# Kernel tuning notes

Hardware: AMD Instinct MI355X
Metric: run time of the kernel (lower is better)

Reference implementation:

```python
import jax, jax.numpy as jnp
import numpy as np
from jax import lax

D_MODEL = 1024
D_STATE = 128
D_CONV = 4
EXPAND = 2
HEADDIM = 64
D_INNER = EXPAND * D_MODEL          # 2048
NHEADS = D_INNER // HEADDIM         # 32
D_IN_PROJ = 2 * D_INNER + 2 * D_STATE + NHEADS  # 4384 (z, xBC, dt)
CONV_CH = D_INNER + 2 * D_STATE     # 2304
CHUNK = 128
EPS = 1e-5
BATCH, SEQ = 2, 2048


def silu(x):
    return x * jax.nn.sigmoid(x)


def rmsnorm(x, w):
    return x * lax.rsqrt(jnp.mean(x * x, axis=-1, keepdims=True) + EPS) * w


def segsum(a):
    # a: (b,h,c,q) -> (b,h,c,q,q); [i,j] = sum_{j<k<=i} a_k, -inf above diag
    q = a.shape[-1]
    cs = jnp.cumsum(a, axis=-1)
    seg = cs[..., :, None] - cs[..., None, :]
    mask = jnp.tril(jnp.ones((q, q), dtype=bool))
    return jnp.where(mask, seg, -jnp.inf)


def ssd(xh, dt, A, B, C):
    # xh: (b,l,h,p), dt: (b,l,h), A: (h,), B,C: (b,l,n). Chunked SSD scan.
    b, l, h, p = xh.shape
    n = B.shape[-1]
    c = l // CHUNK
    X = (xh * dt[..., None]).reshape(b, c, CHUNK, h, p)
    Adt = (A * dt).reshape(b, c, CHUNK, h).transpose(0, 3, 1, 2)  # (b,h,c,q)
    Bc = B.reshape(b, c, CHUNK, n)
    Cc = C.reshape(b, c, CHUNK, n)
    Acs = jnp.cumsum(Adt, axis=-1)
    L = jnp.exp(segsum(Adt))  # (b,h,c,q,q) causal decay within chunk
    Y_diag = jnp.einsum('bcln,bcsn,bhcls,bcshp->bclhp', Cc, Bc, L, X)
    decay_states = jnp.exp(Acs[..., -1:] - Acs)
    states = jnp.einsum('bcln,bhcl,bclhp->bchpn', Bc, decay_states, X)
    chunk_decay = jnp.exp(Acs[..., -1])  # (b,h,c)

    def step(s, inp):
        st, cd = inp
        return s * cd[:, :, None, None] + st, s

    init = jnp.zeros((b, h, p, n), dtype=xh.dtype)
    _, prev = lax.scan(step, init,
                       (states.transpose(1, 0, 2, 3, 4), chunk_decay.transpose(2, 0, 1)))
    # prev: (c,b,h,p,n) = state at start of each chunk
    Y_off = jnp.einsum('bcln,cbhpn,bhcl->bclhp', Cc, prev, jnp.exp(Acs))
    return (Y_diag + Y_off).reshape(b, l, h, p)


def mamba2(x, in_w, conv_w, conv_b, dt_bias, A_log, D, gnorm_w, out_w):
    b, l, _ = x.shape
    zxbcdt = x @ in_w.T  # (b,l,D_IN_PROJ)
    z = zxbcdt[..., :D_INNER]
    xBC = zxbcdt[..., D_INNER:D_INNER + CONV_CH]
    dt = jax.nn.softplus(zxbcdt[..., D_INNER + CONV_CH:] + dt_bias)  # (b,l,h)
    # causal depthwise conv1d
    xp = jnp.pad(xBC, ((0, 0), (D_CONV - 1, 0), (0, 0)))
    conv = sum(xp[:, k:k + l, :] * conv_w[:, k] for k in range(D_CONV)) + conv_b
    xBC = silu(conv)
    xs = xBC[..., :D_INNER]
    B = xBC[..., D_INNER:D_INNER + D_STATE]
    C = xBC[..., D_INNER + D_STATE:]
    A = -jnp.exp(A_log)
    xh = xs.reshape(b, l, NHEADS, HEADDIM)
    y = ssd(xh, dt, A, B, C) + xh * D[None, None, :, None]
    y = y.reshape(b, l, D_INNER)
    y = rmsnorm(y * silu(z), gnorm_w)  # RMSNormGated
    return y @ out_w.T


def setup_inputs() -> dict:
    key = jax.random.key(0)
    ks = jax.random.split(key, 24)
    d = {}
    d['x'] = jax.random.normal(ks[0], (BATCH, SEQ, D_MODEL), dtype=jnp.float32)
    d['norm_w'] = jnp.ones((D_MODEL,), jnp.float32)
    d['out_w_blk'] = jax.random.normal(ks[1], (D_MODEL, 2 * D_MODEL), jnp.float32) * 0.02
    d['out_b_blk'] = jnp.zeros((D_MODEL,), jnp.float32)
    for i, pfx in enumerate(['f_', 'b_']):
        o = 2 + i * 10
        d[pfx + 'in_w'] = jax.random.normal(ks[o], (D_IN_PROJ, D_MODEL), jnp.float32) * 0.02
        d[pfx + 'conv_w'] = jax.random.normal(ks[o + 1], (CONV_CH, D_CONV), jnp.float32) * 0.2
        d[pfx + 'conv_b'] = jnp.zeros((CONV_CH,), jnp.float32)
        d[pfx + 'dt_bias'] = jax.random.normal(ks[o + 2], (NHEADS,), jnp.float32) * 0.1
        d[pfx + 'A_log'] = jnp.log(jax.random.uniform(ks[o + 3], (NHEADS,), jnp.float32, 1.0, 16.0))
        d[pfx + 'D'] = jnp.ones((NHEADS,), jnp.float32)
        d[pfx + 'gnorm_w'] = jnp.ones((D_INNER,), jnp.float32)
        d[pfx + 'out_w'] = jax.random.normal(ks[o + 4], (D_MODEL, D_INNER), jnp.float32) * 0.02
    return d


def reference(x, norm_w, out_w_blk, out_b_blk,
              f_in_w, f_conv_w, f_conv_b, f_dt_bias, f_A_log, f_D, f_gnorm_w, f_out_w,
              b_in_w, b_conv_w, b_conv_b, b_dt_bias, b_A_log, b_D, b_gnorm_w, b_out_w):
    xn = rmsnorm(x, norm_w)
    y_fwd = mamba2(xn, f_in_w, f_conv_w, f_conv_b, f_dt_bias, f_A_log, f_D, f_gnorm_w, f_out_w)
    y_bwd = jnp.flip(
        mamba2(jnp.flip(xn, axis=1), b_in_w, b_conv_w, b_conv_b, b_dt_bias, b_A_log, b_D, b_gnorm_w, b_out_w),
        axis=1)
    out = jnp.concatenate([y_fwd, y_bwd], axis=-1) @ out_w_blk.T + out_b_blk
    return x + out
```

## Files before the change

kernel.cpp:

```cpp
#include <hip/hip_runtime.h>
#include <hip/hip_bf16.h>
#include <math.h>

#define BATCH 2
#define SEQL 2048
#define T 4096
#define DMODEL 1024
#define DINNER 2048
#define DSTATE 128
#define NH 32
#define HD 64
#define DPROJ2 4352
#define CONVCH 2304
#define NCH 16
#define CHUNK 128
#define EPS 1e-5f

#define N_INW ((size_t)DPROJ2 * DMODEL)
#define N_OUTW ((size_t)DMODEL * DINNER)
#define N_ST ((size_t)BATCH * NCH * NH * HD * DSTATE)
#define F2B_BLOCKS 10752
#define TW_BLOCKS 1024

typedef unsigned short u16;
typedef __bf16 bf16x8 __attribute__((ext_vector_type(8)));
typedef float f32x4 __attribute__((ext_vector_type(4)));

__device__ __forceinline__ u16 f2b(float f) {
    union { float f; unsigned u; } v; v.f = f;
    unsigned r = v.u + 0x7fffu + ((v.u >> 16) & 1u);
    return (u16)(r >> 16);
}
__device__ __forceinline__ float b2f(u16 b) {
    union { unsigned u; float f; } v; v.u = ((unsigned)b) << 16;
    return v.f;
}
__device__ __forceinline__ int flipseq(int r) {
    return (r & ~(SEQL - 1)) | ((SEQL - 1) - (r & (SEQL - 1)));
}
__device__ __forceinline__ void gload16(const u16* g, u16* l) {
    __builtin_amdgcn_global_load_lds(
        (const __attribute__((address_space(1))) void*)g,
        (__attribute__((address_space(3))) void*)l, 16, 0, 0);
}

__device__ __forceinline__ float blockReduceSum(float v) {
    __shared__ float red_[4];
    for (int off = 32; off > 0; off >>= 1) v += __shfl_down(v, off);
    int lane = threadIdx.x & 63, wid = threadIdx.x >> 6;
    if (lane == 0) red_[wid] = v;
    __syncthreads();
    if (threadIdx.x == 0) {
        float s = 0.f;
        int nw = blockDim.x >> 6;
        for (int i = 0; i < nw; ++i) s += red_[i];
        red_[0] = s;
    }
    __syncthreads();
    return red_[0];
}

__global__ __launch_bounds__(256) void k_rmsnorm(
    const float* __restrict__ x, const float* __restrict__ w,
    u16* __restrict__ outb)
{
    int row = blockIdx.x;
    const float* xr = x + (size_t)row * DMODEL;
    float ss = 0.f;
    for (int i = threadIdx.x; i < DMODEL; i += 256) { float v = xr[i]; ss += v * v; }
    float tot = blockReduceSum(ss);
    float sc = rsqrtf(tot / DMODEL + EPS);
    for (int i = threadIdx.x; i < DMODEL; i += 256)
        outb[(size_t)row * DMODEL + i] = f2b(xr[i] * sc * w[i]);
}

__global__ __launch_bounds__(256) void k_wprep(
    const float* __restrict__ f_in_w, const float* __restrict__ b_in_w,
    const float* __restrict__ out_w_blk,
    const float* __restrict__ f_out_w, const float* __restrict__ b_out_w,
    u16* __restrict__ d_inwb, u16* __restrict__ d_owbb, u16* __restrict__ d_fowT)
{
    __shared__ u16 t[64][65];
    int bid = blockIdx.x;
    if (bid < F2B_BLOCKS) {
        size_t i = ((size_t)bid * 256 + threadIdx.x) * 4;
        const float* s; u16* d; size_t off;
        if (i < 2 * N_INW) {
            int dir = i >= N_INW;
            off = i - (size_t)dir * N_INW;
            s = dir ? b_in_w : f_in_w; d = d_inwb + (size_t)dir * N_INW;
        } else {
            off = i - 2 * N_INW;
            if (off >= N_OUTW) return;
            s = out_w_blk; d = d_owbb;
        }
        float4 v = *(const float4*)(s + off);
        ushort4 o;
        o.x = f2b(v.x); o.y = f2b(v.y); o.z = f2b(v.z); o.w = f2b(v.w);
        *(ushort4*)(d + off) = o;
        return;
    }
    int b2 = bid - F2B_BLOCKS;
    int dir = b2 >> 9;
    int rem = b2 & 511;
    int c0 = (rem & 31) * 64, e0 = (rem >> 5) * 64;
    const float* src = dir ? b_out_w : f_out_w;
    u16* d = d_fowT + (size_t)dir * N_OUTW;
    for (int i = threadIdx.x; i < 64 * 16; i += 256) {
        int el = i >> 4, c4 = (i & 15) * 4;
        float4 v = *(const float4*)(src + (size_t)(e0 + el) * DINNER + c0 + c4);
        t[c4 + 0][el] = f2b(v.x); t[c4 + 1][el] = f2b(v.y);
        t[c4 + 2][el] = f2b(v.z); t[c4 + 3][el] = f2b(v.w);
    }
    __syncthreads();
    for (int i = threadIdx.x; i < 64 * 16; i += 256) {
        int cl = i >> 4, e4 = (i & 15) * 4;
        ushort4 o;
        o.x = t[cl][e4]; o.y = t[cl][e4 + 1]; o.z = t[cl][e4 + 2]; o.w = t[cl][e4 + 3];
        *(ushort4*)(d + (size_t)(c0 + cl) * DMODEL + e0 + e4) = o;
    }
}

__global__ __launch_bounds__(256, 4) void k_mm_in(
    const u16* __restrict__ A, const u16* __restrict__ W0,
    u16* __restrict__ zb0, u16* __restrict__ xbcraw0)
{
    const int K = DMODEL;
    int dir = blockIdx.z;
    const u16* W = W0 + (size_t)dir * N_INW;
    int m0 = blockIdx.x * 128, n0 = blockIdx.y * 128;

    u16* Cout;
    int ldcc, nbase;
    if (n0 < DINNER) {
        Cout = zb0 + (size_t)dir * T * DINNER;
        ldcc = DINNER;
        nbase = n0;
    } else {
        Cout = xbcraw0 + (size_t)dir * T * CONVCH;
        ldcc = CONVCH;
        nbase = n0 - DINNER;
    }

    __shared__ u16 As[2 * 128 * 32];
    __shared__ u16 Bs[2 * 128 * 32];
    int tid = threadIdx.x;
    int lane = tid & 63;
    int wrow = ((tid >> 6) & 1) * 64, wcol = (tid >> 7) * 64;

    int srow = tid >> 2, skof = (tid & 3) * 8;
    int ar1 = m0 + srow, ar2 = ar1 + 64;
    if (dir) { ar1 = flipseq(ar1); ar2 = flipseq(ar2); }
    const u16* ga1 = A + (size_t)ar1 * K + skof;
    const u16* ga2 = A + (size_t)ar2 * K + skof;
    const u16* gb1 = W + (size_t)(n0 + srow) * K + skof;
    const u16* gb2 = gb1 + (size_t)64 * K;
    u16* la1 = As + tid * 8;
    u16* la2 = As + 2048 + tid * 8;
    u16* lb1 = Bs + tid * 8;
    u16* lb2 = Bs + 2048 + tid * 8;

    int aoff[4], boff[4];
    #pragma unroll
    for (int i = 0; i < 4; ++i) {
        aoff[i] = (wrow + i * 16 + (lane & 15)) * 32 + ((lane >> 4) * 8);
        boff[i] = (wcol + i * 16 + (lane & 15)) * 32 + ((lane >> 4) * 8);
    }

    f32x4 acc[4][4] = {};
    for (int kt = 0; kt < K; kt += 64) {
        gload16(ga1, la1);        gload16(ga2, la2);
        gload16(ga1 + 32, la1 + 4096); gload16(ga2 + 32, la2 + 4096);
        gload16(gb1, lb1);        gload16(gb2, lb2);
        gload16(gb1 + 32, lb1 + 4096); gload16(gb2 + 32, lb2 + 4096);
        ga1 += 64; ga2 += 64; gb1 += 64; gb2 += 64;
        __syncthreads();
        #pragma unroll
        for (int ks = 0; ks < 2; ++ks) {
            bf16x8 af[4], bfv[4];
            #pragma unroll
            for (int i = 0; i < 4; ++i) af[i] = *(const bf16x8*)(As + ks * 4096 + aoff[i]);
            #pragma unroll
            for (int j = 0; j < 4; ++j) bfv[j] = *(const bf16x8*)(Bs + ks * 4096 + boff[j]);
            #pragma unroll
            for (int i = 0; i < 4; ++i)
                #pragma unroll
                for (int j = 0; j < 4; ++j)
                    acc[i][j] = __builtin_amdgcn_mfma_f32_16x16x32_bf16(af[i], bfv[j], acc[i][j], 0, 0, 0);
        }
        __syncthreads();
    }

    int rbase = m0 + wrow + ((lane >> 4) << 2);
    int cbase = nbase + wcol + (lane & 15);
    #pragma unroll
    for (int i = 0; i < 4; ++i)
        #pragma unroll
        for (int j = 0; j < 4; ++j)
            #pragma unroll
            for (int r = 0; r < 4; ++r)
                Cout[(size_t)(rbase + i * 16 + r) * ldcc + cbase + j * 16] = f2b(acc[i][j][r]);
}

__global__ __launch_bounds__(256) void k_mm64(
    const u16* __restrict__ A0, const u16* __restrict__ W0,
    u16* __restrict__ Cb)
{
    int dir = blockIdx.z;
    const u16* A = A0 + dir * DMODEL;
    const u16* W = W0 + (size_t)dir * N_OUTW;

    __shared__ u16 As[2 * 128 * 32];
    __shared__ u16 Bs[2 * 64 * 32];
    int tid = threadIdx.x;
    int lane = tid & 63;
    int w = tid >> 6;
    int m0 = blockIdx.y * 128, n0 = blockIdx.x * 64;
    int wrow = (w & 1) * 64, wcol = (w >> 1) * 32;

    int srow = tid >> 2, skof = (tid & 3) * 8;
    const u16* ga1 = A + (size_t)(m0 + srow) * 2048 + skof;
    const u16* ga2 = A + (size_t)(m0 + 64 + srow) * 2048 + skof;
    const u16* gb  = W + (size_t)(n0 + srow) * DMODEL + skof;
    u16* la1 = As + tid * 8;
    u16* la2 = As + 2048 + tid * 8;
    u16* lb  = Bs + tid * 8;

    int aoff[4], boff[2];
    #pragma unroll
    for (int i = 0; i < 4; ++i)
        aoff[i] = (wrow + i * 16 + (lane & 15)) * 32 + ((lane >> 4) * 8);
    #pragma unroll
    for (int j = 0; j < 2; ++j)
        boff[j] = (wcol + j * 16 + (lane & 15)) * 32 + ((lane >> 4) * 8);

    f32x4 acc[4][2] = {};
    for (int kt = 0; kt < DMODEL; kt += 64) {
        gload16(ga1, la1); gload16(ga1 + 32, la1 + 4096);
        gload16(ga2, la2); gload16(ga2 + 32, la2 + 4096);
        gload16(gb, lb);   gload16(gb + 32, lb + 2048);
        ga1 += 64; ga2 += 64; gb += 64;
        __syncthreads();
        #pragma unroll
        for (int ks = 0; ks < 2; ++ks) {
            bf16x8 af[4], bfv[2];
            #pragma unroll
            for (int i = 0; i < 4; ++i) af[i] = *(const bf16x8*)(As + ks * 4096 + aoff[i]);
            #pragma unroll
            for (int j = 0; j < 2; ++j) bfv[j] = *(const bf16x8*)(Bs + ks * 2048 + boff[j]);
            #pragma unroll
            for (int i = 0; i < 4; ++i)
                #pragma unroll
                for (int j = 0; j < 2; ++j)
                    acc[i][j] = __builtin_amdgcn_mfma_f32_16x16x32_bf16(af[i], bfv[j], acc[i][j], 0, 0, 0);
        }
        __syncthreads();
    }

    int rbase = m0 + wrow + ((lane >> 4) << 2);
    int cbase = n0 + wcol + (lane & 15);
    #pragma unroll
    for (int i = 0; i < 4; ++i)
        #pragma unroll
        for (int j = 0; j < 2; ++j)
            #pragma unroll
            for (int r = 0; r < 4; ++r)
                Cb[(size_t)(rbase + i * 16 + r) * 4096 + dir * 2048 + cbase + j * 16] = f2b(acc[i][j][r]);
}

__global__ __launch_bounds__(256) void k_mm_fin(
    const u16* __restrict__ A1, const u16* __restrict__ A2,
    const u16* __restrict__ W,
    float* __restrict__ out, const float* __restrict__ bias,
    const float* __restrict__ resid)
{
    __shared__ u16 As[4 * 128 * 32];
    __shared__ u16 Bs[2 * 2 * 64 * 32];
    int tid = threadIdx.x;
    int lane = tid & 63;
    int w = tid >> 6;
    int m0 = blockIdx.y * 128, n0 = blockIdx.x * 64;
    int wrow = (w & 1) * 64, wcol = (w >> 1) * 32;

    int srow = tid >> 2, skof = (tid & 3) * 8;
    const u16* ga1  = A1 + (size_t)(m0 + srow) * DINNER + skof;
    const u16* ga1b = A1 + (size_t)(m0 + 64 + srow) * DINNER + skof;
    const u16* ga2  = A2 + (size_t)flipseq(m0 + srow) * DINNER + skof;
    const u16* ga2b = A2 + (size_t)flipseq(m0 + 64 + srow) * DINNER + skof;
    const u16* gb1 = W + (size_t)(n0 + srow) * 4096 + skof;
    const u16* gb2 = gb1 + 2048;
    u16* la1  = As + tid * 8;
    u16* la1b = As + 2048 + tid * 8;
    u16* la2  = As + 8192 + tid * 8;
    u16* la2b = As + 8192 + 2048 + tid * 8;
    u16* lb1 = Bs + tid * 8;
    u16* lb2 = Bs + 4096 + tid * 8;

    int aoff[4], boff[2];
    #pragma unroll
    for (int i = 0; i < 4; ++i)
        aoff[i] = (wrow + i * 16 + (lane & 15)) * 32 + ((lane >> 4) * 8);
    #pragma unroll
    for (int j = 0; j < 2; ++j)
        boff[j] = (wcol + j * 16 + (lane & 15)) * 32 + ((lane >> 4) * 8);

    f32x4 acc[4][2] = {};
    for (int kt = 0; kt < DINNER; kt += 64) {
        gload16(ga1, la1);    gload16(ga1 + 32, la1 + 4096);
        gload16(ga1b, la1b);  gload16(ga1b + 32, la1b + 4096);
        gload16(ga2, la2);    gload16(ga2 + 32, la2 + 4096);
        gload16(ga2b, la2b);  gload16(ga2b + 32, la2b + 4096);
        gload16(gb1, lb1);    gload16(gb1 + 32, lb1 + 2048);
        gload16(gb2, lb2);    gload16(gb2 + 32, lb2 + 2048);
        ga1 += 64; ga1b += 64; ga2 += 64; ga2b += 64; gb1 += 64; gb2 += 64;
        __syncthreads();
        #pragma unroll
        for (int h = 0; h < 2; ++h) {
            #pragma unroll
            for (int ks = 0; ks < 2; ++ks) {
                bf16x8 af[4], bfv[2];
                #pragma unroll
                for (int i = 0; i < 4; ++i)
                    af[i] = *(const bf16x8*)(As + h * 8192 + ks * 4096 + aoff[i]);
                #pragma unroll
                for (int j = 0; j < 2; ++j)
                    bfv[j] = *(const bf16x8*)(Bs + h * 4096 + ks * 2048 + boff[j]);
                #pragma unroll
                for (int i = 0; i < 4; ++i)
                    #pragma unroll
                    for (int j = 0; j < 2; ++j)
                        acc[i][j] = __builtin_amdgcn_mfma_f32_16x16x32_bf16(af[i], bfv[j], acc[i][j], 0, 0, 0);
            }
        }
        __syncthreads();
    }

    int rbase = m0 + wrow + ((lane >> 4) << 2);
    int cbase = n0 + wcol + (lane & 15);
    #pragma unroll
    for (int i = 0; i < 4; ++i)
        #pragma unroll
        for (int j = 0; j < 2; ++j)
            #pragma unroll
            for (int r = 0; r < 4; ++r) {
                int row = rbase + i * 16 + r, col = cbase + j * 16;
                out[(size_t)row * DMODEL + col] =
                    acc[i][j][r] + bias[col] + resid[(size_t)row * DMODEL + col];
            }
}

__global__ __launch_bounds__(256) void k_dt2(
    const u16* __restrict__ xnb,
    const float* __restrict__ inw_f, const float* __restrict__ inw_b,
    const float* __restrict__ dtb_f, const float* __restrict__ dtb_b,
    float* __restrict__ dt)
{
    int dir = blockIdx.z;
    const float* wbase = dir ? inw_b : inw_f;
    const float* dtbia = dir ? dtb_b : dtb_f;
    float* dtp = dt + (size_t)dir * T * NH;

    int r0 = blockIdx.x * 4;
    __shared__ float xs[4][1024];
    int tid = threadIdx.x;
    #pragma unroll
    for (int rr = 0; rr < 4; ++rr) {
        int src = dir ? flipseq(r0 + rr) : (r0 + rr);
        ushort4 v = *(const ushort4*)(xnb + (size_t)src * DMODEL + tid * 4);
        xs[rr][tid * 4 + 0] = b2f(v.x); xs[rr][tid * 4 + 1] = b2f(v.y);
        xs[rr][tid * 4 + 2] = b2f(v.z); xs[rr][tid * 4 + 3] = b2f(v.w);
    }
    __syncthreads();
    int h = tid >> 3, part = tid & 7;
    const float* w = wbase + (size_t)(DPROJ2 + h) * DMODEL;
    float a0 = 0.f, a1 = 0.f, a2 = 0.f, a3 = 0.f;
    for (int kk = 0; kk < 128; ++kk) {
        int k = part + (kk << 3);
        float wv = w[k];
        a0 += xs[0][k] * wv; a1 += xs[1][k] * wv;
        a2 += xs[2][k] * wv; a3 += xs[3][k] * wv;
    }
    #pragma unroll
    for (int off = 4; off > 0; off >>= 1) {
        a0 += __shfl_down(a0, off, 8); a1 += __shfl_down(a1, off, 8);
        a2 += __shfl_down(a2, off, 8); a3 += __shfl_down(a3, off, 8);
    }
    if (part == 0) {
        float bsh = dtbia[h];
        float vv[4] = {a0, a1, a2, a3};
        #pragma unroll
        for (int rr = 0; rr < 4; ++rr) {
            float v = vv[rr] + bsh;
            dtp[(size_t)(r0 + rr) * NH + h] = (v > 20.f) ? v : log1pf(expf(v));
        }
    }
}

__global__ void k_conv(const u16* __restrict__ xraw0,
                       const float* __restrict__ cw_f, const float* __restrict__ cw_b,
                       const float* __restrict__ cb_f, const float* __restrict__ cb_b,
                       const float* __restrict__ dt0,
                       u16* __restrict__ xbcb0, u16* __restrict__ xdtb0)
{
    int dir = blockIdx.z;
    const u16* xraw = xraw0 + (size_t)dir * T * CONVCH;
    const float* cw = dir ? cw_b : cw_f;
    const float* cb = dir ? cb_b : cb_f;
    const float* dt = dt0 + (size_t)dir * T * NH;
    u16* xbcb = xbcb0 + (size_t)dir * T * CONVCH;
    u16* xdtb = xdtb0 + (size_t)dir * T * DINNER;

    int idx = blockIdx.x * blockDim.x + threadIdx.x;
    if (idx >= (T / 4) * (CONVCH / 8)) return;
    int r4 = idx / (CONVCH / 8);
    int c8 = (idx - r4 * (CONVCH / 8)) * 8;
    int r0 = r4 * 4;
    int t0 = r0 & (SEQL - 1);

    float4 cwv[8];
    #pragma unroll
    for (int j = 0; j < 8; ++j) cwv[j] = *(const float4*)(cw + (size_t)(c8 + j) * 4);
    float acc[4][8];
    {
        float4 c0 = *(const float4*)(cb + c8);
        float4 c1 = *(const float4*)(cb + c8 + 4);
        #pragma unroll
        for (int i = 0; i < 4; ++i) {
            acc[i][0] = c0.x; acc[i][1] = c0.y; acc[i][2] = c0.z; acc[i][3] = c0.w;
            acc[i][4] = c1.x; acc[i][5] = c1.y; acc[i][6] = c1.z; acc[i][7] = c1.w;
        }
    }
    #pragma unroll
    for (int s = 0; s < 7; ++s) {
        int tt = t0 - 3 + s;
        if (tt < 0) continue;
        const u16* src = xraw + (size_t)(r0 - 3 + s) * CONVCH + c8;
        ushort4 v0 = *(const ushort4*)src;
        ushort4 v1 = *(const ushort4*)(src + 4);
        float xv[8] = {b2f(v0.x), b2f(v0.y), b2f(v0.z), b2f(v0.w),
                       b2f(v1.x), b2f(v1.y), b2f(v1.z), b2f(v1.w)};
        #pragma unroll
        for (int i = 0; i < 4; ++i) {
            if (i <= s && i >= s - 3) {
                const int j = s - i;
                #pragma unroll
                for (int ch = 0; ch < 8; ++ch) {
                    float wv = (j == 0) ? cwv[ch].x : (j == 1) ? cwv[ch].y
                             : (j == 2) ? cwv[ch].z : cwv[ch].w;
                    acc[i][ch] += xv[ch] * wv;
                }
            }
        }
    }
    #pragma unroll
    for (int i = 0; i < 4; ++i) {
        int r = r0 + i;
        float sgl[8];
        #pragma unroll
        for (int ch = 0; ch < 8; ++ch) sgl[ch] = acc[i][ch] / (1.f + __expf(-acc[i][ch]));
        ushort4 o0, o1;
        o0.x = f2b(sgl[0]); o0.y = f2b(sgl[1]); o0.z = f2b(sgl[2]); o0.w = f2b(sgl[3]);
        o1.x = f2b(sgl[4]); o1.y = f2b(sgl[5]); o1.z = f2b(sgl[6]); o1.w = f2b(sgl[7]);
        *(ushort4*)(xbcb + (size_t)r * CONVCH + c8) = o0;
        *(ushort4*)(xbcb + (size_t)r * CONVCH + c8 + 4) = o1;
        if (c8 < DINNER) {
            float dv = dt[(size_t)r * NH + (c8 >> 6)];
            ushort4 d0, d1;
            d0.x = f2b(sgl[0] * dv); d0.y = f2b(sgl[1] * dv);
            d0.z = f2b(sgl[2] * dv); d0.w = f2b(sgl[3] * dv);
            d1.x = f2b(sgl[4] * dv); d1.y = f2b(sgl[5] * dv);
            d1.z = f2b(sgl[6] * dv); d1.w = f2b(sgl[7] * dv);
            *(ushort4*)(xdtb + (size_t)r * DINNER + c8) = d0;
            *(ushort4*)(xdtb + (size_t)r * DINNER + c8 + 4) = d1;
        }
    }
}

#define LDW 136
__global__ __launch_bounds__(256) void k_states(
    const u16* __restrict__ xbcb0, const u16* __restrict__ xdtb0,
    const float* __restrict__ dt0,
    const float* __restrict__ Alog_f, const float* __restrict__ Alog_b,
    float* __restrict__ acs0, float* __restrict__ cd0, u16* __restrict__ st0)
{
    int dir = blockIdx.z;
    const u16* xbcb = xbcb0 + (size_t)dir * T * CONVCH;
    const u16* xdtb = xdtb0 + (size_t)dir * T * DINNER;
    const float* dt = dt0 + (size_t)dir * T * NH;
    const float* A_log = dir ? Alog_b : Alog_f;
    float* acs = acs0 + (size_t)dir * BATCH * NH * NCH * CHUNK;
    float* cd = cd0 + (size_t)dir * BATCH * NH * NCH;
    u16* st = st0 + (size_t)dir * N_ST;

    __shared__ u16 Bt[128 * LDW];
    __shared__ u16 Xt[64 * LDW];
    __shared__ float cs[128];
    __shared__ float dec_s[128];
    int tid = threadIdx.x;
    int lane = tid & 63;
    int w = tid >> 6;
    int h = blockIdx.x & 31;
    int bc = blockIdx.x >> 5;
    int c = bc & 15, b = bc >> 4;
    int row0 = b * SEQL + c * CHUNK;

    if (tid < 128) {
        float Ah = -expf(A_log[h]);
        cs[tid] = Ah * dt[(size_t)(row0 + tid) * NH + h];
    }
    for (int i = tid; i < 128 * 16; i += 256) {
        int l = i >> 4, pg = (i & 15) * 4;
        ushort4 v = *(const ushort4*)(xdtb + (size_t)(row0 + l) * DINNER + h * HD + pg);
        Xt[(pg + 0) * LDW + l] = v.x; Xt[(pg + 1) * LDW + l] = v.y;
        Xt[(pg + 2) * LDW + l] = v.z; Xt[(pg + 3) * LDW + l] = v.w;
    }
    __syncthreads();
    for (int off = 1; off < 128; off <<= 1) {
        float tval = 0.f;
        if (tid < 128 && tid >= off) tval = cs[tid - off];
        __syncthreads();
        if (tid < 128) cs[tid] += tval;
        __syncthreads();
    }
    size_t abase = ((size_t)(b * NH + h) * NCH + c) << 7;
    if (tid < 128) acs[abase + tid] = cs[tid];
    float a_last = cs[127];
    if (tid == 127) cd[(b * NH + h) * NCH + c] = expf(a_last);
    if (tid < 128) dec_s[tid] = __expf(a_last - cs[tid]);
    __syncthreads();
    for (int i = tid; i < 128 * 32; i += 256) {
        int l = i >> 5, ng = (i & 31) * 4;
        ushort4 v = *(const ushort4*)(xbcb + (size_t)(row0 + l) * CONVCH + DINNER + ng);
        float d = dec_s[l];
        Bt[(ng + 0) * LDW + l] = f2b(b2f(v.x) * d);
        Bt[(ng + 1) * LDW + l] = f2b(b2f(v.y) * d);
        Bt[(ng + 2) * LDW + l] = f2b(b2f(v.z) * d);
        Bt[(ng + 3) * LDW + l] = f2b(b2f(v.w) * d);
    }
    __syncthreads();
    f32x4 tacc[8] = {};
    for (int kk = 0; kk < 4; ++kk) {
        bf16x8 afs = *(const bf16x8*)(Xt + (w * 16 + (lane & 15)) * LDW
                                      + kk * 32 + (lane >> 4) * 8);
        #pragma unroll
        for (int j = 0; j < 8; ++j) {
            bf16x8 bfs = *(const bf16x8*)(Bt + (j * 16 + (lane & 15)) * LDW
                                          + kk * 32 + (lane >> 4) * 8);
            tacc[j] = __builtin_amdgcn_mfma_f32_16x16x32_bf16(afs, bfs, tacc[j], 0, 0, 0);
        }
    }
    size_t sb = (size_t)blockIdx.x * (HD * DSTATE);
    #pragma unroll
    for (int j = 0; j < 8; ++j)
        #pragma unroll
        for (int r = 0; r < 4; ++r) {
            int p = w * 16 + (lane >> 4) * 4 + r;
            int n = j * 16 + (lane & 15);
            st[sb + (size_t)p * DSTATE + n] = f2b(tacc[j][r]);
        }
}

__global__ void k_scan(u16* __restrict__ st0, const float* __restrict__ cd0)
{
    int i = blockIdx.x * blockDim.x + threadIdx.x;
    if (i >= 2 * BATCH * NH * HD * DSTATE) return;
    int dir = i >> 19;
    int j = i & ((1 << 19) - 1);
    u16* st = st0 + (size_t)dir * N_ST;
    const float* cd = cd0 + (size_t)dir * BATCH * NH * NCH;
    int n = j & 127;
    int rest = j >> 7;
    int p = rest & 63; rest >>= 6;
    int h = rest & 31;
    int b = rest >> 5;
    float s = 0.f;
    for (int c = 0; c < NCH; ++c) {
        size_t idx = ((size_t)((b * NCH + c) * NH + h) * HD + p) * DSTATE + n;
        float v = b2f(st[idx]);
        st[idx] = f2b(s);
        s = s * cd[(b * NH + h) * NCH + c] + v;
    }
}

__global__ __launch_bounds__(256) void k_chunk(
    const u16* __restrict__ xbcb0, const u16* __restrict__ xdtb0,
    const float* __restrict__ acs0, const u16* __restrict__ prev0,
    const float* __restrict__ D_f, const float* __restrict__ D_b,
    u16* __restrict__ y0)
{
    int dir = blockIdx.z;
    const u16* xbcb = xbcb0 + (size_t)dir * T * CONVCH;
    const u16* xdtb = xdtb0 + (size_t)dir * T * DINNER;
    const float* acs = acs0 + (size_t)dir * BATCH * NH * NCH * CHUNK;
    const u16* prev = prev0 + (size_t)dir * N_ST;
    const float* Dp = dir ? D_b : D_f;
    u16* y = y0 + (size_t)dir * T * DINNER;

    __shared__ u16 S0[128 * LDW];
    __shared__ u16 Xt[64 * LDW];
    __shared__ float acs_s[128];
    int tid = threadIdx.x;
    int lane = tid & 63;
    int w = tid >> 6;
    int h = blockIdx.x & 31;
    int bc = blockIdx.x >> 5;
    int c = bc & 15, b = bc >> 4;
    int row0 = b * SEQL + c * CHUNK;

    if (tid < 128)
        acs_s[tid] = acs[(((size_t)(b * NH + h) * NCH + c) << 7) + tid];
    for (int i = tid; i < 128 * 16; i += 256) {
        int s = i >> 4, m8 = (i & 15) * 8;
        *(uint4*)(S0 + s * LDW + m8) =
            *(const uint4*)(xbcb + (size_t)(row0 + s) * CONVCH + DINNER + m8);
    }
    for (int i = tid; i < 128 * 16; i += 256) {
        int l = i >> 4, pg = (i & 15) * 4;
        ushort4 v = *(const ushort4*)(xdtb + (size_t)(row0 + l) * DINNER + h * HD + pg);
        Xt[(pg + 0) * LDW + l] = v.x; Xt[(pg + 1) * LDW + l] = v.y;
        Xt[(pg + 2) * LDW + l] = v.z; Xt[(pg + 3) * LDW + l] = v.w;
    }
    __syncthreads();

    int wrow = (w & 1) * 64, wcol = (w >> 1) * 64;
    const u16* cbase = xbcb + (size_t)row0 * CONVCH + DINNER + DSTATE;
    f32x4 sacc[4][4] = {};
    for (int kk = 0; kk < 4; ++kk) {
        bf16x8 af[4], bfr[4];
        #pragma unroll
        for (int i = 0; i < 4; ++i)
            af[i] = *(const bf16x8*)(cbase + (size_t)(wrow + i * 16 + (lane & 15)) * CONVCH
                                     + kk * 32 + (lane >> 4) * 8);
        #pragma unroll
        for (int j = 0; j < 4; ++j)
            bfr[j] = *(const bf16x8*)(S0 + (wcol + j * 16 + (lane & 15)) * LDW
                                      + kk * 32 + (lane >> 4) * 8);
        #pragma unroll
        for (int i = 0; i < 4; ++i)
            #pragma unroll
            for (int j = 0; j < 4; ++j)
                if (wcol + j * 16 <= wrow + i * 16 + 15)
                    sacc[i][j] = __builtin_amdgcn_mfma_f32_16x16x32_bf16(af[i], bfr[j], sacc[i][j], 0, 0, 0);
    }
    __syncthreads();
    #pragma unroll
    for (int i = 0; i < 4; ++i)
        #pragma unroll
        for (int j = 0; j < 4; ++j) {
            int s = wcol + j * 16 + (lane & 15);
            #pragma unroll
            for (int r = 0; r < 4; ++r) {
                int l = wrow + i * 16 + (lane >> 4) * 4 + r;
                float v = (s <= l) ? sacc[i][j][r] * __expf(acs_s[l] - acs_s[s]) : 0.f;
                S0[l * LDW + s] = f2b(v);
            }
        }
    __syncthreads();
    f32x4 yacc[2][4] = {};
    for (int kk = 0; kk < 4; ++kk) {
        bf16x8 af[2], bfr[4];
        #pragma unroll
        for (int i = 0; i < 2; ++i)
            af[i] = *(const bf16x8*)(S0 + (w * 32 + i * 16 + (lane & 15)) * LDW
                                     + kk * 32 + (lane >> 4) * 8);
        #pragma unroll
        for (int j = 0; j < 4; ++j)
            bfr[j] = *(const bf16x8*)(Xt + (j * 16 + (lane & 15)) * LDW
                                      + kk * 32 + (lane >> 4) * 8);
        #pragma unroll
        for (int i = 0; i < 2; ++i)
            #pragma unroll
            for (int j = 0; j < 4; ++j)
                yacc[i][j] = __builtin_amdgcn_mfma_f32_16x16x32_bf16(af[i], bfr[j], yacc[i][j], 0, 0, 0);
    }
    __syncthreads();
    size_t sb = (size_t)blockIdx.x * (HD * DSTATE);
    for (int i = tid; i < 64 * 16; i += 256) {
        int p = i >> 4, m8 = (i & 15) * 8;
        *(uint4*)(S0 + p * LDW + m8) = *(const uint4*)(prev + sb + (size_t)p * DSTATE + m8);
    }
    __syncthreads();
    f32x4 oacc[2][4] = {};
    for (int kk = 0; kk < 4; ++kk) {
        bf16x8 af[2], bfr[4];
        #pragma unroll
        for (int i = 0; i < 2; ++i)
            af[i] = *(const bf16x8*)(cbase + (size_t)(w * 32 + i * 16 + (lane & 15)) * CONVCH
                                     + kk * 32 + (lane >> 4) * 8);
        #pragma unroll
        for (int j = 0; j < 4; ++j)
            bfr[j] = *(const bf16x8*)(S0 + (j * 16 + (lane & 15)) * LDW
                                      + kk * 32 + (lane >> 4) * 8);
        #pragma unroll
        for (int i = 0; i < 2; ++i)
            #pragma unroll
            for (int j = 0; j < 4; ++j)
                oacc[i][j] = __builtin_amdgcn_mfma_f32_16x16x32_bf16(af[i], bfr[j], oacc[i][j], 0, 0, 0);
    }
    float Dh = Dp[h];
    #pragma unroll
    for (int i = 0; i < 2; ++i)
        #pragma unroll
        for (int j = 0; j < 4; ++j)
            #pragma unroll
            for (int r = 0; r < 4; ++r) {
                int l = w * 32 + i * 16 + (lane >> 4) * 4 + r;
                int p = j * 16 + (lane & 15);
                float val = yacc[i][j][r] + __expf(acs_s[l]) * oacc[i][j][r]
                          + b2f(xbcb[(size_t)(row0 + l) * CONVCH + h * HD + p]) * Dh;
                y[(size_t)(row0 + l) * DINNER + h * HD + p] = f2b(val);
            }
}

__global__ __launch_bounds__(256) void k_gate(
    const u16* __restrict__ y0, const u16* __restrict__ zb0,
    const float* __restrict__ gw_f, const float* __restrict__ gw_b,
    u16* __restrict__ out0)
{
    int dir = blockIdx.z;
    const u16* y = y0 + (size_t)dir * T * DINNER;
    const u16* zb = zb0 + (size_t)dir * T * DINNER;
    const float* gw = dir ? gw_b : gw_f;
    u16* out = out0 + (size_t)dir * T * DINNER;

    int r = blockIdx.x;
    int tid = threadIdx.x;
    float tv[8];
    float ss = 0.f;
    #pragma unroll
    for (int it = 0; it < 2; ++it) {
        int i = (it * 256 + tid) * 4;
        ushort4 yv = *(const ushort4*)(y + (size_t)r * DINNER + i);
        ushort4 zv = *(const ushort4*)(zb + (size_t)r * DINNER + i);
        float z0 = b2f(zv.x), z1 = b2f(zv.y), z2 = b2f(zv.z), z3 = b2f(zv.w);
        float t0 = b2f(yv.x) * (z0 / (1.f + __expf(-z0)));
        float t1 = b2f(yv.y) * (z1 / (1.f + __expf(-z1)));
        float t2 = b2f(yv.z) * (z2 / (1.f + __expf(-z2)));
        float t3 = b2f(yv.w) * (z3 / (1.f + __expf(-z3)));
        tv[it * 4 + 0] = t0; tv[it * 4 + 1] = t1; tv[it * 4 + 2] = t2; tv[it * 4 + 3] = t3;
        ss += t0 * t0 + t1 * t1 + t2 * t2 + t3 * t3;
    }
    float tot = blockReduceSum(ss);
    float sc = rsqrtf(tot / DINNER + EPS);
    #pragma unroll
    for (int it = 0; it < 2; ++it) {
        int i = (it * 256 + tid) * 4;
        ushort4 o;
        o.x = f2b(tv[it * 4 + 0] * sc * gw[i]);
        o.y = f2b(tv[it * 4 + 1] * sc * gw[i + 1]);
        o.z = f2b(tv[it * 4 + 2] * sc * gw[i + 2]);
        o.w = f2b(tv[it * 4 + 3] * sc * gw[i + 3]);
        *(ushort4*)(out + (size_t)r * DINNER + i) = o;
    }
}

extern "C" void kernel_launch(void* const* d_in, const int* in_sizes, int n_in,
                              void* d_out, int out_size, void* d_ws, size_t ws_size,
                              hipStream_t stream)
{
    const float* x         = (const float*)d_in[0];
    const float* norm_w    = (const float*)d_in[1];
    const float* out_w_blk = (const float*)d_in[2];
    const float* out_b_blk = (const float*)d_in[3];
    const float* f_in_w    = (const float*)d_in[4];
    const float* f_conv_w  = (const float*)d_in[5];
    const float* f_conv_b  = (const float*)d_in[6];
    const float* f_dt_bias = (const float*)d_in[7];
    const float* f_A_log   = (const float*)d_in[8];
    const float* f_D       = (const float*)d_in[9];
    const float* f_gnorm_w = (const float*)d_in[10];
    const float* f_out_w   = (const float*)d_in[11];
    const float* b_in_w    = (const float*)d_in[12];
    const float* b_conv_w  = (const float*)d_in[13];
    const float* b_conv_b  = (const float*)d_in[14];
    const float* b_dt_bias = (const float*)d_in[15];
    const float* b_A_log   = (const float*)d_in[16];
    const float* b_D       = (const float*)d_in[17];
    const float* b_gnorm_w = (const float*)d_in[18];
    const float* b_out_w   = (const float*)d_in[19];
    float* out = (float*)d_out;

    char* ws = (char*)d_ws;
    u16*  xnb    = (u16*)ws;   ws += (size_t)T * DMODEL * 2;
    u16*  zb     = (u16*)ws;   ws += (size_t)2 * T * DINNER * 2;
    u16*  xbcraw = (u16*)ws;   ws += (size_t)2 * T * CONVCH * 2;
    u16*  xbcb   = (u16*)ws;   ws += (size_t)2 * T * CONVCH * 2;
    u16*  xdtb   = (u16*)ws;   ws += (size_t)2 * T * DINNER * 2;
    float* dtb   = (float*)ws; ws += (size_t)2 * T * NH * 4;
    float* acs   = (float*)ws; ws += (size_t)2 * BATCH * NH * NCH * CHUNK * 4;
    float* cd    = (float*)ws; ws += (size_t)2 * BATCH * NH * NCH * 4;
    u16*  stb    = (u16*)ws;   ws += (size_t)2 * N_ST * 2;
    u16*  inwb   = (u16*)ws;   ws += (size_t)2 * N_INW * 2;
    u16*  fowT2  = (u16*)ws;   ws += (size_t)2 * N_OUTW * 2;
    u16*  owbb   = (u16*)ws;   ws += (size_t)N_OUTW * 2;
    u16*  yb16  = xbcraw;
    u16*  ybb   = xdtb;
    u16*  Mcomb = xbcb;

    k_rmsnorm<<<T, 256, 0, stream>>>(x, norm_w, xnb);
    k_wprep<<<F2B_BLOCKS + TW_BLOCKS, 256, 0, stream>>>(
        f_in_w, b_in_w, out_w_blk, f_out_w, b_out_w, inwb, owbb, fowT2);

    {
        dim3 g(T / 128, DPROJ2 / 128, 2);
        k_mm_in<<<g, 256, 0, stream>>>(xnb, inwb, zb, xbcraw);
    }
    {
        dim3 g(T / 4, 1, 2);
        k_dt2<<<g, 256, 0, stream>>>(xnb, f_in_w, b_in_w, f_dt_bias, b_dt_bias, dtb);
    }
    {
        dim3 g(((T / 4) * (CONVCH / 8) + 255) / 256, 1, 2);
        k_conv<<<g, 256, 0, stream>>>(xbcraw, f_conv_w, b_conv_w, f_conv_b, b_conv_b,
                                      dtb, xbcb, xdtb);
    }
    {
        dim3 g(BATCH * NCH * NH, 1, 2);
        k_states<<<g, 256, 0, stream>>>(xbcb, xdtb, dtb, f_A_log, b_A_log, acs, cd, stb);
    }
    k_scan<<<(2 * BATCH * NH * HD * DSTATE) / 256, 256, 0, stream>>>(stb, cd);
    {
        dim3 g(BATCH * NCH * NH, 1, 2);
        k_chunk<<<g, 256, 0, stream>>>(xbcb, xdtb, acs, stb, f_D, b_D, yb16);
    }
    {
        dim3 g(T, 1, 2);
        k_gate<<<g, 256, 0, stream>>>(yb16, zb, f_gnorm_w, b_gnorm_w, ybb);
    }
    {
        dim3 g(DINNER / 64, DMODEL / 128, 2);
        k_mm64<<<g, 256, 0, stream>>>(owbb, fowT2, Mcomb);
    }
    {
        dim3 g(DMODEL / 64, T / 128, 1);
        k_mm_fin<<<g, 256, 0, stream>>>(ybb, ybb + (size_t)T * DINNER, Mcomb,
                                        out, out_b_blk, x);
    }
}
```

Before: 513.1 us.

## Use 256x256 8-wave GEMM for in-projection and fuse dt projection into RMSNorm

Replaces the 128x128 in-projection GEMM with a 256x256 tile, 512-thread kernel. It uses swizzled LDS, direct global-to-LDS loads, a staggered double buffer and setprio around the MFMA bursts. That kernel covers the first 4096 output columns, and the old kernel, given a column offset, handles the remaining 256. The dt projection is folded into the RMSNorm kernel so xn is reused from LDS and one launch is dropped. In exchange there are fewer blocks (512 large tiles) and higher register and LDS pressure.

```diff
diff --git a/kernel.cpp b/kernel.cpp
--- a/kernel.cpp
+++ b/kernel.cpp
@@ -44,6 +44,8 @@
         (__attribute__((address_space(3))) void*)l, 16, 0, 0);
 }
 
+#define FENCE asm volatile("" ::: "memory")
+
 __device__ __forceinline__ float blockReduceSum(float v) {
     __shared__ float red_[4];
     for (int off = 32; off > 0; off >>= 1) v += __shfl_down(v, off);
@@ -60,18 +62,70 @@
     return red_[0];
 }
 
-__global__ __launch_bounds__(256) void k_rmsnorm(
+__global__ __launch_bounds__(256) void k_rmsdt(
     const float* __restrict__ x, const float* __restrict__ w,
-    u16* __restrict__ outb)
-{
-    int row = blockIdx.x;
+    const float* __restrict__ inw_f, const float* __restrict__ inw_b,
+    const float* __restrict__ dtb_f, const float* __restrict__ dtb_b,
+    u16* __restrict__ outb, float* __restrict__ dt)
+{
+    __shared__ float xs[4][1024];
+    int r0 = blockIdx.x * 4;
+    int tid = threadIdx.x;
+    int lane = tid & 63, wv = tid >> 6;
+    int row = r0 + wv;
     const float* xr = x + (size_t)row * DMODEL;
+    float4 v[4];
     float ss = 0.f;
-    for (int i = threadIdx.x; i < DMODEL; i += 256) { float v = xr[i]; ss += v * v; }
-    float tot = blockReduceSum(ss);
-    float sc = rsqrtf(tot / DMODEL + EPS);
-    for (int i = threadIdx.x; i < DMODEL; i += 256)
-        outb[(size_t)row * DMODEL + i] = f2b(xr[i] * sc * w[i]);
+    #pragma unroll
+    for (int i = 0; i < 4; ++i) {
+        v[i] = *(const float4*)(xr + (i * 64 + lane) * 4);
+        ss += v[i].x * v[i].x + v[i].y * v[i].y + v[i].z * v[i].z + v[i].w * v[i].w;
+    }
+    #pragma unroll
+    for (int off = 32; off > 0; off >>= 1) ss += __shfl_down(ss, off);
+    ss = __shfl(ss, 0);
+    float sc = rsqrtf(ss / DMODEL + EPS);
+    #pragma unroll
+    for (int i = 0; i < 4; ++i) {
+        int c = (i * 64 + lane) * 4;
+        float4 wv4 = *(const float4*)(w + c);
+        ushort4 o;
+        o.x = f2b(v[i].x * sc * wv4.x);
+        o.y = f2b(v[i].y * sc * wv4.y);
+        o.z = f2b(v[i].z * sc * wv4.z);
+        o.w = f2b(v[i].w * sc * wv4.w);
+        *(ushort4*)(outb + (size_t)row * DMODEL + c) = o;
+        xs[wv][c + 0] = b2f(o.x); xs[wv][c + 1] = b2f(o.y);
+        xs[wv][c + 2] = b2f(o.z); xs[wv][c + 3] = b2f(o.w);
+    }
+    __syncthreads();
+    int h2 = tid >> 2, part = tid & 3;
+    int dir = h2 >> 5, h = h2 & 31;
+    const float* wd = (dir ? inw_b : inw_f) + (size_t)(DPROJ2 + h) * DMODEL;
+    float a0 = 0.f, a1 = 0.f, a2 = 0.f, a3 = 0.f;
+    for (int kk = 0; kk < 256; ++kk) {
+        int k = part + (kk << 2);
+        float wvv = wd[k];
+        a0 += xs[0][k] * wvv; a1 += xs[1][k] * wvv;
+        a2 += xs[2][k] * wvv; a3 += xs[3][k] * wvv;
+    }
+    #pragma unroll
+    for (int off = 2; off > 0; off >>= 1) {
+        a0 += __shfl_down(a0, off, 4); a1 += __shfl_down(a1, off, 4);
+        a2 += __shfl_down(a2, off, 4); a3 += __shfl_down(a3, off, 4);
+    }
+    if (part == 0) {
+        float bsh = dir ? dtb_b[h] : dtb_f[h];
+        float* dtp = dt + (size_t)dir * T * NH;
+        float vv[4] = {a0, a1, a2, a3};
+        #pragma unroll
+        for (int rr = 0; rr < 4; ++rr) {
+            int rg = r0 + rr;
+            if (dir) rg = flipseq(rg);
+            float vvv = vv[rr] + bsh;
+            dtp[(size_t)rg * NH + h] = (vvv > 20.f) ? vvv : log1pf(expf(vvv));
+        }
+    }
 }
 
 __global__ __launch_bounds__(256) void k_wprep(
@@ -121,14 +175,138 @@
     }
 }
 
+__global__ __launch_bounds__(512, 2) void k_mm_in8(
+    const u16* __restrict__ A, const u16* __restrict__ W0,
+    u16* __restrict__ zb0, u16* __restrict__ xbcraw0)
+{
+    __shared__ u16 lds_[8 * 8192];
+    int dir = blockIdx.z;
+    const u16* W = W0 + (size_t)dir * N_INW;
+    int m0 = blockIdx.x * 256, n0 = blockIdx.y * 256;
+
+    u16* Cout; int ldcc, nbase;
+    if (n0 < DINNER) {
+        Cout = zb0 + (size_t)dir * T * DINNER;
+        ldcc = DINNER;
+        nbase = n0;
+    } else {
+        Cout = xbcraw0 + (size_t)dir * T * CONVCH;
+        ldcc = CONVCH;
+        nbase = n0 - DINNER;
+    }
+
+    int tid = threadIdx.x;
+    int lane = tid & 63;
+    int w = tid >> 6;
+    int wm = w >> 2;
+    int wn = w & 3;
+    int l15 = lane & 15;
+    int gsw0 = (((lane >> 4) ^ (lane & 7)) << 3);
+    int gsw1 = (((4 + (lane >> 4)) ^ (lane & 7)) << 3);
+
+    const u16* pA[2][2];
+    const u16* pB[2][2];
+    int swz = ((lane & 7) ^ (lane >> 3)) << 3;
+    #pragma unroll
+    for (int h = 0; h < 2; ++h)
+        #pragma unroll
+        for (int c = 0; c < 2; ++c) {
+            int rl = (w * 2 + c) * 8 + (lane >> 3);
+            int grow = m0 + h * 128 + rl;
+            if (dir) grow = flipseq(grow);
+            pA[h][c] = A + (size_t)grow * DMODEL + swz;
+            pB[h][c] = W + (size_t)(n0 + h * 128 + rl) * DMODEL + swz;
+        }
+    int dst0 = (w * 2 + 0) * 512 + lane * 8;
+    int dst1 = (w * 2 + 1) * 512 + lane * 8;
+
+#define STAGE_A(t_, h_) do { \
+        gload16(pA[h_][0] + (t_) * 64, lds_ + (((t_) & 1) * 4 + (h_)) * 8192 + dst0); \
+        gload16(pA[h_][1] + (t_) * 64, lds_ + (((t_) & 1) * 4 + (h_)) * 8192 + dst1); \
+    } while (0)
+#define STAGE_B(t_, h_) do { \
+        gload16(pB[h_][0] + (t_) * 64, lds_ + (((t_) & 1) * 4 + 2 + (h_)) * 8192 + dst0); \
+        gload16(pB[h_][1] + (t_) * 64, lds_ + (((t_) & 1) * 4 + 2 + (h_)) * 8192 + dst1); \
+    } while (0)
+
+    f32x4 acc[8][4] = {};
+    bf16x8 bfv[4][2];
+
+    STAGE_A(0, 0); STAGE_A(0, 1); STAGE_B(0, 0); STAGE_B(0, 1);
+    FENCE;
+    STAGE_B(1, 0); STAGE_B(1, 1);
+    asm volatile("s_waitcnt vmcnt(4)" ::: "memory");
+    __builtin_amdgcn_s_barrier();
+    FENCE;
+
+    for (int kt = 0; kt < 16; ++kt) {
+        int d = kt & 1;
+        const u16* Ab = lds_ + (d * 4 + wm) * 8192;
+        const u16* Bb = lds_ + (d * 4 + 2 + (wn >> 1)) * 8192;
+        int nrow0 = (wn & 1) * 64;
+        #pragma unroll
+        for (int q = 0; q < 4; ++q) {
+            if (q == 0) {
+                #pragma unroll
+                for (int j = 0; j < 4; ++j) {
+                    const u16* bp = Bb + (nrow0 + j * 16 + l15) * 64;
+                    bfv[j][0] = *(const bf16x8*)(bp + gsw0);
+                    bfv[j][1] = *(const bf16x8*)(bp + gsw1);
+                }
+            }
+            const u16* ap0 = Ab + ((q * 2 + 0) * 16 + l15) * 64;
+            const u16* ap1 = Ab + ((q * 2 + 1) * 16 + l15) * 64;
+            bf16x8 a0k0 = *(const bf16x8*)(ap0 + gsw0);
+            bf16x8 a0k1 = *(const bf16x8*)(ap0 + gsw1);
+            bf16x8 a1k0 = *(const bf16x8*)(ap1 + gsw0);
+            bf16x8 a1k1 = *(const bf16x8*)(ap1 + gsw1);
+            if (q == 0)      { if (kt < 15) STAGE_A(kt + 1, 0); }
+            else if (q == 1) { if (kt < 15) STAGE_A(kt + 1, 1); }
+            else if (q == 2) { if (kt < 14) STAGE_B(kt + 2, 0); }
+            else             { if (kt < 14) STAGE_B(kt + 2, 1); }
+            FENCE;
+            __builtin_amdgcn_s_barrier();
+            asm volatile("s_waitcnt lgkmcnt(0)" ::: "memory");
+            __builtin_amdgcn_s_setprio(1);
+            #pragma unroll
+            for (int j = 0; j < 4; ++j) {
+                acc[q * 2 + 0][j] = __builtin_amdgcn_mfma_f32_16x16x32_bf16(a0k0, bfv[j][0], acc[q * 2 + 0][j], 0, 0, 0);
+                acc[q * 2 + 0][j] = __builtin_amdgcn_mfma_f32_16x16x32_bf16(a0k1, bfv[j][1], acc[q * 2 + 0][j], 0, 0, 0);
+                acc[q * 2 + 1][j] = __builtin_amdgcn_mfma_f32_16x16x32_bf16(a1k0, bfv[j][0], acc[q * 2 + 1][j], 0, 0, 0);
+                acc[q * 2 + 1][j] = __builtin_amdgcn_mfma_f32_16x16x32_bf16(a1k1, bfv[j][1], acc[q * 2 + 1][j], 0, 0, 0);
+            }
+            __builtin_amdgcn_s_setprio(0);
+            if (q == 3) {
+                if (kt < 14)       asm volatile("s_waitcnt vmcnt(4)" ::: "memory");
+                else if (kt == 14) asm volatile("s_waitcnt vmcnt(0)" ::: "memory");
+            }
+            FENCE;
+            __builtin_amdgcn_s_barrier();
+            FENCE;
+        }
+    }
+#undef STAGE_A
+#undef STAGE_B
+
+    int rb = m0 + wm * 128 + ((lane >> 4) << 2);
+    int cb = nbase + wn * 64 + l15;
+    #pragma unroll
+    for (int i = 0; i < 8; ++i)
+        #pragma unroll
+        for (int j = 0; j < 4; ++j)
+            #pragma unroll
+            for (int r = 0; r < 4; ++r)
+                Cout[(size_t)(rb + i * 16 + r) * ldcc + cb + j * 16] = f2b(acc[i][j][r]);
+}
+
 __global__ __launch_bounds__(256, 4) void k_mm_in(
     const u16* __restrict__ A, const u16* __restrict__ W0,
-    u16* __restrict__ zb0, u16* __restrict__ xbcraw0)
+    u16* __restrict__ zb0, u16* __restrict__ xbcraw0, int ny0)
 {
     const int K = DMODEL;
     int dir = blockIdx.z;
     const u16* W = W0 + (size_t)dir * N_INW;
-    int m0 = blockIdx.x * 128, n0 = blockIdx.y * 128;
+    int m0 = blockIdx.x * 128, n0 = (blockIdx.y + ny0) * 128;
 
     u16* Cout;
     int ldcc, nbase;
@@ -347,53 +525,6 @@
                 out[(size_t)row * DMODEL + col] =
                     acc[i][j][r] + bias[col] + resid[(size_t)row * DMODEL + col];
             }
-}
-
-__global__ __launch_bounds__(256) void k_dt2(
-    const u16* __restrict__ xnb,
-    const float* __restrict__ inw_f, const float* __restrict__ inw_b,
-    const float* __restrict__ dtb_f, const float* __restrict__ dtb_b,
-    float* __restrict__ dt)
-{
-    int dir = blockIdx.z;
-    const float* wbase = dir ? inw_b : inw_f;
-    const float* dtbia = dir ? dtb_b : dtb_f;
-    float* dtp = dt + (size_t)dir * T * NH;
-
-    int r0 = blockIdx.x * 4;
-    __shared__ float xs[4][1024];
-    int tid = threadIdx.x;
-    #pragma unroll
-    for (int rr = 0; rr < 4; ++rr) {
-        int src = dir ? flipseq(r0 + rr) : (r0 + rr);
-        ushort4 v = *(const ushort4*)(xnb + (size_t)src * DMODEL + tid * 4);
-        xs[rr][tid * 4 + 0] = b2f(v.x); xs[rr][tid * 4 + 1] = b2f(v.y);
-        xs[rr][tid * 4 + 2] = b2f(v.z); xs[rr][tid * 4 + 3] = b2f(v.w);
-    }
-    __syncthreads();
-    int h = tid >> 3, part = tid & 7;
-    const float* w = wbase + (size_t)(DPROJ2 + h) * DMODEL;
-    float a0 = 0.f, a1 = 0.f, a2 = 0.f, a3 = 0.f;
-    for (int kk = 0; kk < 128; ++kk) {
-        int k = part + (kk << 3);
-        float wv = w[k];
-        a0 += xs[0][k] * wv; a1 += xs[1][k] * wv;
-        a2 += xs[2][k] * wv; a3 += xs[3][k] * wv;
-    }
-    #pragma unroll
-    for (int off = 4; off > 0; off >>= 1) {
-        a0 += __shfl_down(a0, off, 8); a1 += __shfl_down(a1, off, 8);
-        a2 += __shfl_down(a2, off, 8); a3 += __shfl_down(a3, off, 8);
-    }
-    if (part == 0) {
-        float bsh = dtbia[h];
-        float vv[4] = {a0, a1, a2, a3};
-        #pragma unroll
-        for (int rr = 0; rr < 4; ++rr) {
-            float v = vv[rr] + bsh;
-            dtp[(size_t)(r0 + rr) * NH + h] = (v > 20.f) ? v : log1pf(expf(v));
-        }
-    }
 }
 
 __global__ void k_conv(const u16* __restrict__ xraw0,
@@ -797,17 +928,18 @@
     u16*  ybb   = xdtb;
     u16*  Mcomb = xbcb;
 
-    k_rmsnorm<<<T, 256, 0, stream>>>(x, norm_w, xnb);
+    k_rmsdt<<<T / 4, 256, 0, stream>>>(x, norm_w, f_in_w, b_in_w,
+                                       f_dt_bias, b_dt_bias, xnb, dtb);
     k_wprep<<<F2B_BLOCKS + TW_BLOCKS, 256, 0, stream>>>(
         f_in_w, b_in_w, out_w_blk, f_out_w, b_out_w, inwb, owbb, fowT2);
 
     {
-        dim3 g(T / 128, DPROJ2 / 128, 2);
-        k_mm_in<<<g, 256, 0, stream>>>(xnb, inwb, zb, xbcraw);
+        dim3 g(T / 256, 16, 2);
+        k_mm_in8<<<g, 512, 0, stream>>>(xnb, inwb, zb, xbcraw);
     }
     {
-        dim3 g(T / 4, 1, 2);
-        k_dt2<<<g, 256, 0, stream>>>(xnb, f_in_w, b_in_w, f_dt_bias, b_dt_bias, dtb);
+        dim3 g(T / 128, 2, 2);
+        k_mm_in<<<g, 256, 0, stream>>>(xnb, inwb, zb, xbcraw, 32);
     }
     {
         dim3 g(((T / 4) * (CONVCH / 8) + 255) / 256, 1, 2);
```

New measurement: 509.6 us. About the same (-0.7%).
